# Kernel tuning notes

Hardware: AMD Instinct MI355X
Metric: run time of the kernel (lower is better)

The kernel has to match this reference:

```python
import jax, jax.numpy as jnp
import numpy as np

B, K, DIM = 8192, 256, 1024


def setup_inputs() -> dict:
    key = jax.random.key(0)
    k1, k2, k3 = jax.random.split(key, 3)
    x = jax.random.normal(k1, (B, DIM), dtype=jnp.float32)
    centers = jax.random.uniform(k2, (K, DIM), dtype=jnp.float32)
    # torch init: D = 0.2 * rand + 0.9
    D = 0.2 * jax.random.uniform(k3, (K, DIM), dtype=jnp.float32) + 0.9
    return {"x": x, "centers": centers, "D": D}


def reference(x, centers, D):
    # Per-class axis-aligned (diagonal) covariance
    D_abs = jnp.abs(D) + 1e-4                      # [K, DIM]
    D_inv = 1.0 / D_abs                            # [K, DIM]
    log_det = jnp.sum(jnp.log(D_abs), axis=1)      # [K]
    det_scale_factor = -0.5 * log_det
    det_scale_safe = jnp.exp(det_scale_factor - jnp.max(det_scale_factor))  # [K]

    # dist_sq[b,k] = sum_d (x[b,d]-c[k,d])^2 * D_inv[k,d]
    # Expanded quadratic form avoids materializing the [B,K,DIM] diff tensor.
    x2 = jnp.einsum('bd,kd->bk', x * x, D_inv)             # [B, K]
    xc = jnp.einsum('bd,kd->bk', x, centers * D_inv)       # [B, K]
    c2 = jnp.sum(centers * centers * D_inv, axis=1)        # [K]
    dist_sq = x2 - 2.0 * xc + c2[None, :]                  # [B, K]

    # Gaussian path (isCauchy=False)
    expo = -0.5 * dist_sq
    expo_safe = expo - jnp.max(expo, axis=-1, keepdims=True)
    numer_safe = det_scale_safe[None, :] * jnp.exp(expo_safe)
    denom_safe = jnp.sum(numer_safe, axis=1, keepdims=True)
    resp = numer_safe / denom_safe                         # [B, K]
    return resp
```

## Files before the change

### kernel.cpp

```cpp
#include <hip/hip_runtime.h>

typedef _Float16 f16x8 __attribute__((ext_vector_type(8)));
typedef _Float16 f16x4 __attribute__((ext_vector_type(4)));
typedef float f32x4 __attribute__((ext_vector_type(4)));

#define B_N 8192
#define K_N 256
#define DIM_N 1024

__global__ __launch_bounds__(256) void prep_w(const float* __restrict__ Dm,
                                              const float* __restrict__ Cm,
                                              _Float16* __restrict__ Upk,
                                              _Float16* __restrict__ Wpk,
                                              float* __restrict__ ec) {
    const int k = blockIdx.x, t = threadIdx.x;
    const int d = t * 4;
    const float4 dv = *(const float4*)(Dm + (size_t)k * DIM_N + d);
    const float4 cv = *(const float4*)(Cm + (size_t)k * DIM_N + d);
    float dd[4] = {dv.x, dv.y, dv.z, dv.w};
    float cc[4] = {cv.x, cv.y, cv.z, cv.w};
    f16x4 uo, wo;
    float llog = 0.f, lc2 = 0.f;
#pragma unroll
    for (int i = 0; i < 4; ++i) {
        float da = fabsf(dd[i]) + 1e-4f;
        float dinv = 1.0f / da;
        llog += logf(da);
        lc2 += cc[i] * cc[i] * dinv;
        uo[i] = (_Float16)(dinv - 1.0f);
        wo[i] = (_Float16)(-2.0f * cc[i] * dinv);
    }
    const int cg = k >> 4, cl = k & 15;
    const int kc = d >> 5, g = (d >> 3) & 3, j0 = d & 7;
    const size_t off = ((size_t)(cg * 32 + kc) * 64 + g * 16 + cl) * 8 + j0;
    *(f16x4*)(Upk + off) = uo;
    *(f16x4*)(Wpk + off) = wo;
    float both = llog + lc2;
#pragma unroll
    for (int m = 1; m <= 32; m <<= 1) both += __shfl_xor(both, m, 64);
    __shared__ float sb[4];
    if ((t & 63) == 0) sb[t >> 6] = both;
    __syncthreads();
    if (t == 0) ec[k] = -0.5f * (sb[0] + sb[1] + sb[2] + sb[3]);
}

__global__ __launch_bounds__(256, 1)
void gmm_gemm(const float* __restrict__ x,
              const _Float16* __restrict__ Upk,
              const _Float16* __restrict__ Wpk,
              float* __restrict__ S) {
    __shared__ __align__(16) char lds[32768];

    const int tid = threadIdx.x;
    const int wave = tid >> 6, lane = tid & 63;
    const int l15 = lane & 15, g4 = lane >> 4;
    const int wr = wave >> 1, wc = wave & 1;
    const int bid = blockIdx.x;
    const int rowp = bid >> 1, colp = bid & 1;
    const int bRow = rowp * 64, bCol = colp * 128;

    const int xr = lane >> 3, xdq = lane & 7;
    const float* xp = x + (size_t)(bRow + wr * 32 + xr) * DIM_N + xdq * 4;

    const int cgb = colp * 8 + wc * 4;
    const _Float16* upb = Upk + (size_t)cgb * 32 * 512 + lane * 8;
    const _Float16* wpb = Wpk + (size_t)cgb * 32 * 512 + lane * 8;

    char* wlds = lds + wave * 8192;
    const int di = xdq >> 1, jb = (lane & 1) * 8;
    int awr[4];
#pragma unroll
    for (int i = 0; i < 4; ++i) {
        const int r = xr + 8 * i;
        awr[i] = ((r >> 4) << 10) + (((r & 15) + (di << 4)) << 4) + jb;
    }

    float4 xv[3][4];
    f16x8 ub[2][4], wb[2][4];
    f32x4 acc[2][4];
#pragma unroll
    for (int m = 0; m < 2; ++m)
#pragma unroll
        for (int n = 0; n < 4; ++n) { f32x4 z = {0.f, 0.f, 0.f, 0.f}; acc[m][n] = z; }

    auto issueB = [&](int bank, int c) {
#pragma unroll
        for (int n = 0; n < 4; ++n) {
            ub[bank][n] = *(const f16x8*)(upb + ((size_t)n * 32 + c) * 512);
            wb[bank][n] = *(const f16x8*)(wpb + ((size_t)n * 32 + c) * 512);
        }
    };
    auto issueX = [&](int slot, int c) {
#pragma unroll
        for (int i = 0; i < 4; ++i)
            xv[slot][i] = *(const float4*)(xp + (size_t)c * 32 + (size_t)i * 8 * DIM_N);
    };
    auto stageA = [&](int sel, int slot) {
        char* base = wlds + sel * 4096;
#pragma unroll
        for (int i = 0; i < 4; ++i) {
            const float f0 = xv[slot][i].x, f1 = xv[slot][i].y;
            const float f2 = xv[slot][i].z, f3 = xv[slot][i].w;
            f16x4 h2 = {(_Float16)(f0 * f0), (_Float16)(f1 * f1),
                        (_Float16)(f2 * f2), (_Float16)(f3 * f3)};
            f16x4 hx = {(_Float16)f0, (_Float16)f1, (_Float16)f2, (_Float16)f3};
            *(f16x4*)(base + awr[i]) = h2;
            *(f16x4*)(base + 2048 + awr[i]) = hx;
        }
    };
    auto compute = [&](int sel, int bank) {
        char* base = wlds + sel * 4096;
        f16x8 a2f[2], axf[2];
#pragma unroll
        for (int m = 0; m < 2; ++m) {
            a2f[m] = *(const f16x8*)(base + m * 1024 + lane * 16);
            axf[m] = *(const f16x8*)(base + 2048 + m * 1024 + lane * 16);
        }
        __builtin_amdgcn_s_setprio(1);
#pragma unroll
        for (int m = 0; m < 2; ++m)
#pragma unroll
            for (int n = 0; n < 4; ++n) {
                acc[m][n] = __builtin_amdgcn_mfma_f32_16x16x32_f16(a2f[m], ub[bank][n], acc[m][n], 0, 0, 0);
                acc[m][n] = __builtin_amdgcn_mfma_f32_16x16x32_f16(axf[m], wb[bank][n], acc[m][n], 0, 0, 0);
            }
        __builtin_amdgcn_s_setprio(0);
    };

    issueB(0, 0);
    issueX(0, 0); issueX(1, 1); issueX(2, 2);
    stageA(0, 0);

#pragma unroll
    for (int c = 0; c < 32; ++c) {
        const int sel = c & 1;
        if (c < 31) issueB(sel ^ 1, c + 1);
        if (c < 29) issueX((c + 3) % 3, c + 3);
        if (c < 31) stageA(sel ^ 1, (c + 1) % 3);
        compute(sel, sel);
    }

#pragma unroll
    for (int m = 0; m < 2; ++m) {
        const int rb = bRow + wr * 32 + m * 16 + g4 * 4;
#pragma unroll
        for (int n = 0; n < 4; ++n) {
            const int cb = bCol + wc * 64 + n * 16 + l15;
#pragma unroll
            for (int j = 0; j < 4; ++j)
                S[(size_t)(rb + j) * K_N + cb] = acc[m][n][j];
        }
    }
}

__global__ __launch_bounds__(256)
void gmm_soft(float* __restrict__ S, const float* __restrict__ ecg) {
    const int tid = threadIdx.x;
    const int wave = tid >> 6, lane = tid & 63;
    const int r = blockIdx.x * 4 + wave;
    const int k0 = lane * 4;
    float4 s = *(const float4*)(S + (size_t)r * K_N + k0);
    float4 cv = *(const float4*)(ecg + k0);
    float e[4] = {fmaf(-0.5f, s.x, cv.x), fmaf(-0.5f, s.y, cv.y),
                  fmaf(-0.5f, s.z, cv.z), fmaf(-0.5f, s.w, cv.w)};
    float m = fmaxf(fmaxf(e[0], e[1]), fmaxf(e[2], e[3]));
#pragma unroll
    for (int msk = 1; msk <= 32; msk <<= 1) m = fmaxf(m, __shfl_xor(m, msk, 64));
    float p[4], sum = 0.f;
#pragma unroll
    for (int j = 0; j < 4; ++j) {
        p[j] = __expf(e[j] - m);
        sum += p[j];
    }
#pragma unroll
    for (int msk = 1; msk <= 32; msk <<= 1) sum += __shfl_xor(sum, msk, 64);
    const float inv = 1.0f / sum;
    *(float4*)(S + (size_t)r * K_N + k0) = make_float4(p[0] * inv, p[1] * inv, p[2] * inv, p[3] * inv);
}

extern "C" void kernel_launch(void* const* d_in, const int* in_sizes, int n_in,
                              void* d_out, int out_size, void* d_ws, size_t ws_size,
                              hipStream_t stream) {
    const float* x = (const float*)d_in[0];
    const float* cen = (const float*)d_in[1];
    const float* Dm = (const float*)d_in[2];
    float* out = (float*)d_out;

    char* ws = (char*)d_ws;
    _Float16* Upk = (_Float16*)(ws);
    _Float16* Wpk = (_Float16*)(ws + 524288);
    float* ec = (float*)(ws + 1048576);

    prep_w<<<dim3(K_N), dim3(256), 0, stream>>>(Dm, cen, Upk, Wpk, ec);
    gmm_gemm<<<dim3(256), dim3(256), 0, stream>>>(x, Upk, Wpk, out);
    gmm_soft<<<dim3(B_N / 4), dim3(256), 0, stream>>>(out, ec);
}
```

Baseline: 36.25 us.

## Fuse GEMM and softmax into one kernel with full-row tiles per block

```diff
diff --git a/kernel.cpp b/kernel.cpp
--- a/kernel.cpp
+++ b/kernel.cpp
@@ -44,138 +44,195 @@
     if (t == 0) ec[k] = -0.5f * (sb[0] + sb[1] + sb[2] + sb[3]);
 }
 
-__global__ __launch_bounds__(256, 1)
-void gmm_gemm(const float* __restrict__ x,
-              const _Float16* __restrict__ Upk,
-              const _Float16* __restrict__ Wpk,
-              float* __restrict__ S) {
-    __shared__ __align__(16) char lds[32768];
+__global__ __launch_bounds__(512, 1)
+void gmm_fused(const float* __restrict__ x,
+               const _Float16* __restrict__ Upk,
+               const _Float16* __restrict__ Wpk,
+               const float* __restrict__ ecg,
+               float* __restrict__ out) {
+    __shared__ __align__(16) char lds[16384];
+    __shared__ float red[8][32];
 
     const int tid = threadIdx.x;
     const int wave = tid >> 6, lane = tid & 63;
     const int l15 = lane & 15, g4 = lane >> 4;
-    const int wr = wave >> 1, wc = wave & 1;
-    const int bid = blockIdx.x;
-    const int rowp = bid >> 1, colp = bid & 1;
-    const int bRow = rowp * 64, bCol = colp * 128;
-
-    const int xr = lane >> 3, xdq = lane & 7;
-    const float* xp = x + (size_t)(bRow + wr * 32 + xr) * DIM_N + xdq * 4;
-
-    const int cgb = colp * 8 + wc * 4;
-    const _Float16* upb = Upk + (size_t)cgb * 32 * 512 + lane * 8;
-    const _Float16* wpb = Wpk + (size_t)cgb * 32 * 512 + lane * 8;
-
-    char* wlds = lds + wave * 8192;
-    const int di = xdq >> 1, jb = (lane & 1) * 8;
-    int awr[4];
-#pragma unroll
-    for (int i = 0; i < 4; ++i) {
-        const int r = xr + 8 * i;
-        awr[i] = ((r >> 4) << 10) + (((r & 15) + (di << 4)) << 4) + jb;
-    }
-
-    float4 xv[3][4];
-    f16x8 ub[2][4], wb[2][4];
-    f32x4 acc[2][4];
-#pragma unroll
-    for (int m = 0; m < 2; ++m)
-#pragma unroll
-        for (int n = 0; n < 4; ++n) { f32x4 z = {0.f, 0.f, 0.f, 0.f}; acc[m][n] = z; }
-
+    const int bRow = blockIdx.x * 32;
+
+    const int srow = tid >> 4, sdg = tid & 15;
+    const float* xp = x + (size_t)(bRow + srow) * DIM_N + sdg * 4;
+    const int wByte = srow * 128 + ((((sdg >> 1) ^ (srow & 7)) << 4) | ((sdg & 1) << 3));
+
+    const _Float16* upb = Upk + (size_t)(wave * 2) * 32 * 512 + lane * 8;
+    const _Float16* wpb = Wpk + (size_t)(wave * 2) * 32 * 512 + lane * 8;
+
+    int aRd[2][2];
+#pragma unroll
+    for (int m = 0; m < 2; ++m)
+#pragma unroll
+        for (int k2 = 0; k2 < 2; ++k2) {
+            const int row = m * 16 + l15;
+            aRd[m][k2] = row * 128 + ((((k2 * 4 + g4) ^ (row & 7)) << 4));
+        }
+
+    f32x4 acc[2][2];
+#pragma unroll
+    for (int m = 0; m < 2; ++m)
+#pragma unroll
+        for (int n = 0; n < 2; ++n) { f32x4 z = {0.f, 0.f, 0.f, 0.f}; acc[m][n] = z; }
+
+    float4 xv[6];
+    f16x8 ub[2][2][2], wb[2][2][2];
+
+    auto issueX = [&](int slot, int c) { xv[slot] = *(const float4*)(xp + c * 64); };
     auto issueB = [&](int bank, int c) {
 #pragma unroll
-        for (int n = 0; n < 4; ++n) {
-            ub[bank][n] = *(const f16x8*)(upb + ((size_t)n * 32 + c) * 512);
-            wb[bank][n] = *(const f16x8*)(wpb + ((size_t)n * 32 + c) * 512);
-        }
+        for (int n = 0; n < 2; ++n)
+#pragma unroll
+            for (int k2 = 0; k2 < 2; ++k2) {
+                const int kc = c * 2 + k2;
+                ub[bank][n][k2] = *(const f16x8*)(upb + (size_t)(n * 32 + kc) * 512);
+                wb[bank][n][k2] = *(const f16x8*)(wpb + (size_t)(n * 32 + kc) * 512);
+            }
     };
-    auto issueX = [&](int slot, int c) {
-#pragma unroll
-        for (int i = 0; i < 4; ++i)
-            xv[slot][i] = *(const float4*)(xp + (size_t)c * 32 + (size_t)i * 8 * DIM_N);
-    };
-    auto stageA = [&](int sel, int slot) {
-        char* base = wlds + sel * 4096;
-#pragma unroll
-        for (int i = 0; i < 4; ++i) {
-            const float f0 = xv[slot][i].x, f1 = xv[slot][i].y;
-            const float f2 = xv[slot][i].z, f3 = xv[slot][i].w;
-            f16x4 h2 = {(_Float16)(f0 * f0), (_Float16)(f1 * f1),
-                        (_Float16)(f2 * f2), (_Float16)(f3 * f3)};
-            f16x4 hx = {(_Float16)f0, (_Float16)f1, (_Float16)f2, (_Float16)f3};
-            *(f16x4*)(base + awr[i]) = h2;
-            *(f16x4*)(base + 2048 + awr[i]) = hx;
-        }
+    auto stage = [&](int sel, int slot) {
+        char* base = lds + sel * 8192;
+        const float f0 = xv[slot].x, f1 = xv[slot].y, f2 = xv[slot].z, f3 = xv[slot].w;
+        f16x4 h2 = {(_Float16)(f0 * f0), (_Float16)(f1 * f1),
+                    (_Float16)(f2 * f2), (_Float16)(f3 * f3)};
+        f16x4 hx = {(_Float16)f0, (_Float16)f1, (_Float16)f2, (_Float16)f3};
+        *(f16x4*)(base + wByte) = h2;
+        *(f16x4*)(base + 4096 + wByte) = hx;
     };
     auto compute = [&](int sel, int bank) {
-        char* base = wlds + sel * 4096;
-        f16x8 a2f[2], axf[2];
-#pragma unroll
-        for (int m = 0; m < 2; ++m) {
-            a2f[m] = *(const f16x8*)(base + m * 1024 + lane * 16);
-            axf[m] = *(const f16x8*)(base + 2048 + m * 1024 + lane * 16);
-        }
+        char* base = lds + sel * 8192;
+        f16x8 a2f[2][2], axf[2][2];
+#pragma unroll
+        for (int m = 0; m < 2; ++m)
+#pragma unroll
+            for (int k2 = 0; k2 < 2; ++k2) {
+                a2f[m][k2] = *(const f16x8*)(base + aRd[m][k2]);
+                axf[m][k2] = *(const f16x8*)(base + 4096 + aRd[m][k2]);
+            }
         __builtin_amdgcn_s_setprio(1);
 #pragma unroll
         for (int m = 0; m < 2; ++m)
 #pragma unroll
-            for (int n = 0; n < 4; ++n) {
-                acc[m][n] = __builtin_amdgcn_mfma_f32_16x16x32_f16(a2f[m], ub[bank][n], acc[m][n], 0, 0, 0);
-                acc[m][n] = __builtin_amdgcn_mfma_f32_16x16x32_f16(axf[m], wb[bank][n], acc[m][n], 0, 0, 0);
-            }
+            for (int n = 0; n < 2; ++n)
+#pragma unroll
+                for (int k2 = 0; k2 < 2; ++k2) {
+                    acc[m][n] = __builtin_amdgcn_mfma_f32_16x16x32_f16(a2f[m][k2], ub[bank][n][k2], acc[m][n], 0, 0, 0);
+                    acc[m][n] = __builtin_amdgcn_mfma_f32_16x16x32_f16(axf[m][k2], wb[bank][n][k2], acc[m][n], 0, 0, 0);
+                }
         __builtin_amdgcn_s_setprio(0);
     };
 
     issueB(0, 0);
-    issueX(0, 0); issueX(1, 1); issueX(2, 2);
-    stageA(0, 0);
-
-#pragma unroll
-    for (int c = 0; c < 32; ++c) {
+    issueB(1, 1);
+#pragma unroll
+    for (int s = 0; s < 6; ++s) issueX(s, s);
+    stage(0, 0);
+    asm volatile("s_waitcnt lgkmcnt(0)" ::: "memory");
+    __builtin_amdgcn_s_barrier();
+    __builtin_amdgcn_sched_barrier(0);
+
+#pragma unroll
+    for (int c = 0; c < 16; ++c) {
         const int sel = c & 1;
-        if (c < 31) issueB(sel ^ 1, c + 1);
-        if (c < 29) issueX((c + 3) % 3, c + 3);
-        if (c < 31) stageA(sel ^ 1, (c + 1) % 3);
+        if (c < 10) issueX(c % 6, c + 6);
+        if (c < 15) stage(sel ^ 1, (c + 1) % 6);
         compute(sel, sel);
-    }
-
-#pragma unroll
-    for (int m = 0; m < 2; ++m) {
-        const int rb = bRow + wr * 32 + m * 16 + g4 * 4;
-#pragma unroll
-        for (int n = 0; n < 4; ++n) {
-            const int cb = bCol + wc * 64 + n * 16 + l15;
+        if (c < 14) issueB(sel, c + 2);
+        if (c < 15) {
+            asm volatile("s_waitcnt lgkmcnt(0)" ::: "memory");
+            __builtin_amdgcn_s_barrier();
+            __builtin_amdgcn_sched_barrier(0);
+        }
+    }
+
+    const int cls0 = wave * 32 + l15;
+    const float ecv[2] = {ecg[cls0], ecg[cls0 + 16]};
+
+    float e[2][2][4];
+#pragma unroll
+    for (int m = 0; m < 2; ++m)
+#pragma unroll
+        for (int n = 0; n < 2; ++n)
 #pragma unroll
             for (int j = 0; j < 4; ++j)
-                S[(size_t)(rb + j) * K_N + cb] = acc[m][n][j];
-        }
-    }
-}
-
-__global__ __launch_bounds__(256)
-void gmm_soft(float* __restrict__ S, const float* __restrict__ ecg) {
-    const int tid = threadIdx.x;
-    const int wave = tid >> 6, lane = tid & 63;
-    const int r = blockIdx.x * 4 + wave;
-    const int k0 = lane * 4;
-    float4 s = *(const float4*)(S + (size_t)r * K_N + k0);
-    float4 cv = *(const float4*)(ecg + k0);
-    float e[4] = {fmaf(-0.5f, s.x, cv.x), fmaf(-0.5f, s.y, cv.y),
-                  fmaf(-0.5f, s.z, cv.z), fmaf(-0.5f, s.w, cv.w)};
-    float m = fmaxf(fmaxf(e[0], e[1]), fmaxf(e[2], e[3]));
-#pragma unroll
-    for (int msk = 1; msk <= 32; msk <<= 1) m = fmaxf(m, __shfl_xor(m, msk, 64));
-    float p[4], sum = 0.f;
-#pragma unroll
-    for (int j = 0; j < 4; ++j) {
-        p[j] = __expf(e[j] - m);
-        sum += p[j];
-    }
-#pragma unroll
-    for (int msk = 1; msk <= 32; msk <<= 1) sum += __shfl_xor(sum, msk, 64);
-    const float inv = 1.0f / sum;
-    *(float4*)(S + (size_t)r * K_N + k0) = make_float4(p[0] * inv, p[1] * inv, p[2] * inv, p[3] * inv);
+                e[m][n][j] = fmaf(-0.5f, acc[m][n][j], ecv[n]);
+
+    float mx[2][4];
+#pragma unroll
+    for (int m = 0; m < 2; ++m)
+#pragma unroll
+        for (int j = 0; j < 4; ++j) mx[m][j] = fmaxf(e[m][0][j], e[m][1][j]);
+#pragma unroll
+    for (int msk = 1; msk <= 8; msk <<= 1)
+#pragma unroll
+        for (int m = 0; m < 2; ++m)
+#pragma unroll
+            for (int j = 0; j < 4; ++j)
+                mx[m][j] = fmaxf(mx[m][j], __shfl_xor(mx[m][j], msk, 64));
+    if (l15 == 0) {
+#pragma unroll
+        for (int m = 0; m < 2; ++m)
+#pragma unroll
+            for (int j = 0; j < 4; ++j) red[wave][m * 16 + g4 * 4 + j] = mx[m][j];
+    }
+    __syncthreads();
+    float gm[2][4];
+#pragma unroll
+    for (int m = 0; m < 2; ++m)
+#pragma unroll
+        for (int j = 0; j < 4; ++j) {
+            const int r = m * 16 + g4 * 4 + j;
+            float v = red[0][r];
+#pragma unroll
+            for (int w = 1; w < 8; ++w) v = fmaxf(v, red[w][r]);
+            gm[m][j] = v;
+        }
+    __syncthreads();
+
+    float p[2][2][4], sm[2][4];
+#pragma unroll
+    for (int m = 0; m < 2; ++m)
+#pragma unroll
+        for (int j = 0; j < 4; ++j) sm[m][j] = 0.f;
+#pragma unroll
+    for (int m = 0; m < 2; ++m)
+#pragma unroll
+        for (int n = 0; n < 2; ++n)
+#pragma unroll
+            for (int j = 0; j < 4; ++j) {
+                p[m][n][j] = __expf(e[m][n][j] - gm[m][j]);
+                sm[m][j] += p[m][n][j];
+            }
+#pragma unroll
+    for (int msk = 1; msk <= 8; msk <<= 1)
+#pragma unroll
+        for (int m = 0; m < 2; ++m)
+#pragma unroll
+            for (int j = 0; j < 4; ++j) sm[m][j] += __shfl_xor(sm[m][j], msk, 64);
+    if (l15 == 0) {
+#pragma unroll
+        for (int m = 0; m < 2; ++m)
+#pragma unroll
+            for (int j = 0; j < 4; ++j) red[wave][m * 16 + g4 * 4 + j] = sm[m][j];
+    }
+    __syncthreads();
+#pragma unroll
+    for (int m = 0; m < 2; ++m)
+#pragma unroll
+        for (int j = 0; j < 4; ++j) {
+            const int r = m * 16 + g4 * 4 + j;
+            float t = red[0][r];
+#pragma unroll
+            for (int w = 1; w < 8; ++w) t += red[w][r];
+            const float inv = 1.0f / t;
+#pragma unroll
+            for (int n = 0; n < 2; ++n)
+                out[(size_t)(bRow + r) * K_N + cls0 + n * 16] = p[m][n][j] * inv;
+        }
 }
 
 extern "C" void kernel_launch(void* const* d_in, const int* in_sizes, int n_in,
@@ -192,6 +249,5 @@
     float* ec = (float*)(ws + 1048576);
 
     prep_w<<<dim3(K_N), dim3(256), 0, stream>>>(Dm, cen, Upk, Wpk, ec);
-    gmm_gemm<<<dim3(256), dim3(256), 0, stream>>>(x, Upk, Wpk, out);
-    gmm_soft<<<dim3(B_N / 4), dim3(256), 0, stream>>>(out, ec);
+    gmm_fused<<<dim3(B_N / 32), dim3(512), 0, stream>>>(x, Upk, Wpk, ec, out);
 }
```

Result: faster. 31.79 us (-12.3%).

## Share cooperatively staged x tiles across 8 waves with block-wide LDS pipeline

Applied to the files above, without the earlier changes.

```diff
diff --git a/kernel.cpp b/kernel.cpp
--- a/kernel.cpp
+++ b/kernel.cpp
@@ -44,111 +44,135 @@
     if (t == 0) ec[k] = -0.5f * (sb[0] + sb[1] + sb[2] + sb[3]);
 }
 
-__global__ __launch_bounds__(256, 1)
+__global__ __launch_bounds__(512, 1)
 void gmm_gemm(const float* __restrict__ x,
               const _Float16* __restrict__ Upk,
               const _Float16* __restrict__ Wpk,
               float* __restrict__ S) {
-    __shared__ __align__(16) char lds[32768];
+    __shared__ __align__(16) char xlds[65536];
 
     const int tid = threadIdx.x;
     const int wave = tid >> 6, lane = tid & 63;
     const int l15 = lane & 15, g4 = lane >> 4;
-    const int wr = wave >> 1, wc = wave & 1;
+    const int wr = wave >> 2, wc = wave & 3;
     const int bid = blockIdx.x;
-    const int rowp = bid >> 1, colp = bid & 1;
+    const int rowp = bid & 127, colp = bid >> 7;
     const int bRow = rowp * 64, bCol = colp * 128;
 
-    const int xr = lane >> 3, xdq = lane & 7;
-    const float* xp = x + (size_t)(bRow + wr * 32 + xr) * DIM_N + xdq * 4;
-
-    const int cgb = colp * 8 + wc * 4;
-    const _Float16* upb = Upk + (size_t)cgb * 32 * 512 + lane * 8;
-    const _Float16* wpb = Wpk + (size_t)cgb * 32 * 512 + lane * 8;
-
-    char* wlds = lds + wave * 8192;
-    const int di = xdq >> 1, jb = (lane & 1) * 8;
-    int awr[4];
-#pragma unroll
-    for (int i = 0; i < 4; ++i) {
-        const int r = xr + 8 * i;
-        awr[i] = ((r >> 4) << 10) + (((r & 15) + (di << 4)) << 4) + jb;
-    }
-
-    float4 xv[3][4];
-    f16x8 ub[2][4], wb[2][4];
-    f32x4 acc[2][4];
+    const int sr = tid >> 3, q4 = tid & 7;
+    const float* xq = x + (size_t)(bRow + sr) * DIM_N + q4 * 4;
+    int wAddr[8];
+#pragma unroll
+    for (int j = 0; j < 8; ++j) {
+        const int cl = j >> 1, k2 = j & 1;
+        const int fi = (sr >> 4) * 2 + k2;
+        wAddr[j] = cl * 8192 + fi * 1024 + ((sr & 15) + 16 * (q4 >> 1)) * 16 + (q4 & 1) * 8;
+    }
+
+    const _Float16* upb = Upk + (size_t)(colp * 8 + wc * 2) * 32 * 512 + lane * 8;
+    const _Float16* wpb = Wpk + (size_t)(colp * 8 + wc * 2) * 32 * 512 + lane * 8;
+
+    f32x4 acc[2][2];
 #pragma unroll
     for (int m = 0; m < 2; ++m)
 #pragma unroll
-        for (int n = 0; n < 4; ++n) { f32x4 z = {0.f, 0.f, 0.f, 0.f}; acc[m][n] = z; }
-
+        for (int n = 0; n < 2; ++n) { f32x4 z = {0.f, 0.f, 0.f, 0.f}; acc[m][n] = z; }
+
+    float4 xs[2][8];
+    f16x8 ub[2][2][2], wb[2][2][2];
+
+    auto issueQ = [&](int bank, int q) {
+#pragma unroll
+        for (int j = 0; j < 8; ++j) xs[bank][j] = *(const float4*)(xq + q * 256 + j * 32);
+    };
+    auto writeQ = [&](int bank, int buf) {
+        char* base = xlds + buf * 32768;
+#pragma unroll
+        for (int j = 0; j < 8; ++j) {
+            const float4 v = xs[bank][j];
+            f16x4 h = {(_Float16)v.x, (_Float16)v.y, (_Float16)v.z, (_Float16)v.w};
+            *(f16x4*)(base + wAddr[j]) = h;
+        }
+    };
     auto issueB = [&](int bank, int c) {
 #pragma unroll
-        for (int n = 0; n < 4; ++n) {
-            ub[bank][n] = *(const f16x8*)(upb + ((size_t)n * 32 + c) * 512);
-            wb[bank][n] = *(const f16x8*)(wpb + ((size_t)n * 32 + c) * 512);
-        }
-    };
-    auto issueX = [&](int slot, int c) {
-#pragma unroll
-        for (int i = 0; i < 4; ++i)
-            xv[slot][i] = *(const float4*)(xp + (size_t)c * 32 + (size_t)i * 8 * DIM_N);
-    };
-    auto stageA = [&](int sel, int slot) {
-        char* base = wlds + sel * 4096;
-#pragma unroll
-        for (int i = 0; i < 4; ++i) {
-            const float f0 = xv[slot][i].x, f1 = xv[slot][i].y;
-            const float f2 = xv[slot][i].z, f3 = xv[slot][i].w;
-            f16x4 h2 = {(_Float16)(f0 * f0), (_Float16)(f1 * f1),
-                        (_Float16)(f2 * f2), (_Float16)(f3 * f3)};
-            f16x4 hx = {(_Float16)f0, (_Float16)f1, (_Float16)f2, (_Float16)f3};
-            *(f16x4*)(base + awr[i]) = h2;
-            *(f16x4*)(base + 2048 + awr[i]) = hx;
-        }
-    };
-    auto compute = [&](int sel, int bank) {
-        char* base = wlds + sel * 4096;
-        f16x8 a2f[2], axf[2];
-#pragma unroll
-        for (int m = 0; m < 2; ++m) {
-            a2f[m] = *(const f16x8*)(base + m * 1024 + lane * 16);
-            axf[m] = *(const f16x8*)(base + 2048 + m * 1024 + lane * 16);
-        }
-        __builtin_amdgcn_s_setprio(1);
+        for (int n = 0; n < 2; ++n)
+#pragma unroll
+            for (int k2 = 0; k2 < 2; ++k2) {
+                const int kc = c * 2 + k2;
+                ub[bank][n][k2] = *(const f16x8*)(upb + (size_t)(n * 32 + kc) * 512);
+                wb[bank][n][k2] = *(const f16x8*)(wpb + (size_t)(n * 32 + kc) * 512);
+            }
+    };
+    auto compute = [&](int c, int bank) {
+        const char* base = xlds + ((c >> 2) & 1) * 32768 + (c & 3) * 8192;
+        f16x8 axf[2][2];
 #pragma unroll
         for (int m = 0; m < 2; ++m)
 #pragma unroll
-            for (int n = 0; n < 4; ++n) {
-                acc[m][n] = __builtin_amdgcn_mfma_f32_16x16x32_f16(a2f[m], ub[bank][n], acc[m][n], 0, 0, 0);
-                acc[m][n] = __builtin_amdgcn_mfma_f32_16x16x32_f16(axf[m], wb[bank][n], acc[m][n], 0, 0, 0);
+            for (int k2 = 0; k2 < 2; ++k2) {
+                const int fi = (wr * 2 + m) * 2 + k2;
+                axf[m][k2] = *(const f16x8*)(base + fi * 1024 + lane * 16);
             }
-        __builtin_amdgcn_s_setprio(0);
-    };
-
-    issueB(0, 0);
-    issueX(0, 0); issueX(1, 1); issueX(2, 2);
-    stageA(0, 0);
-
-#pragma unroll
-    for (int c = 0; c < 32; ++c) {
-        const int sel = c & 1;
-        if (c < 31) issueB(sel ^ 1, c + 1);
-        if (c < 29) issueX((c + 3) % 3, c + 3);
-        if (c < 31) stageA(sel ^ 1, (c + 1) % 3);
-        compute(sel, sel);
-    }
+#pragma unroll
+        for (int m = 0; m < 2; ++m)
+#pragma unroll
+            for (int k2 = 0; k2 < 2; ++k2) {
+                const f16x8 a2 = axf[m][k2] * axf[m][k2];
+#pragma unroll
+                for (int n = 0; n < 2; ++n) {
+                    acc[m][n] = __builtin_amdgcn_mfma_f32_16x16x32_f16(a2, ub[bank][n][k2], acc[m][n], 0, 0, 0);
+                    acc[m][n] = __builtin_amdgcn_mfma_f32_16x16x32_f16(axf[m][k2], wb[bank][n][k2], acc[m][n], 0, 0, 0);
+                }
+            }
+    };
+
+    issueB(0, 0); issueB(1, 1);
+    issueQ(0, 0); issueQ(1, 1);
+    writeQ(0, 0);
+    asm volatile("s_waitcnt lgkmcnt(0)" ::: "memory");
+    __builtin_amdgcn_s_barrier();
+    __builtin_amdgcn_sched_barrier(0);
+    writeQ(1, 1);
+    issueQ(0, 2);
+    compute(0, 0);  issueB(0, 2);
+    compute(1, 1);  issueB(1, 3);
+    compute(2, 0);  issueB(0, 4);
+    compute(3, 1);  issueB(1, 5);
+    asm volatile("s_waitcnt lgkmcnt(0)" ::: "memory");
+    __builtin_amdgcn_s_barrier();
+    __builtin_amdgcn_sched_barrier(0);
+    writeQ(0, 0);
+    issueQ(1, 3);
+    compute(4, 0);  issueB(0, 6);
+    compute(5, 1);  issueB(1, 7);
+    compute(6, 0);  issueB(0, 8);
+    compute(7, 1);  issueB(1, 9);
+    asm volatile("s_waitcnt lgkmcnt(0)" ::: "memory");
+    __builtin_amdgcn_s_barrier();
+    __builtin_amdgcn_sched_barrier(0);
+    writeQ(1, 1);
+    compute(8, 0);   issueB(0, 10);
+    compute(9, 1);   issueB(1, 11);
+    compute(10, 0);  issueB(0, 12);
+    compute(11, 1);  issueB(1, 13);
+    asm volatile("s_waitcnt lgkmcnt(0)" ::: "memory");
+    __builtin_amdgcn_s_barrier();
+    __builtin_amdgcn_sched_barrier(0);
+    compute(12, 0);  issueB(0, 14);
+    compute(13, 1);  issueB(1, 15);
+    compute(14, 0);
+    compute(15, 1);
 
 #pragma unroll
     for (int m = 0; m < 2; ++m) {
         const int rb = bRow + wr * 32 + m * 16 + g4 * 4;
-#pragma unroll
-        for (int n = 0; n < 4; ++n) {
-            const int cb = bCol + wc * 64 + n * 16 + l15;
-#pragma unroll
-            for (int j = 0; j < 4; ++j)
-                S[(size_t)(rb + j) * K_N + cb] = acc[m][n][j];
+        const int cb = bCol + wc * 32 + l15;
+#pragma unroll
+        for (int j = 0; j < 4; ++j) {
+            float* p = S + (size_t)(rb + j) * K_N + cb;
+            p[0] = acc[m][0][j];
+            p[16] = acc[m][1][j];
         }
     }
 }
@@ -192,6 +216,6 @@
     float* ec = (float*)(ws + 1048576);
 
     prep_w<<<dim3(K_N), dim3(256), 0, stream>>>(Dm, cen, Upk, Wpk, ec);
-    gmm_gemm<<<dim3(256), dim3(256), 0, stream>>>(x, Upk, Wpk, out);
+    gmm_gemm<<<dim3(256), dim3(512), 0, stream>>>(x, Upk, Wpk, out);
     gmm_soft<<<dim3(B_N / 4), dim3(256), 0, stream>>>(out, ec);
 }
```

Result: faster. 32.65 us (-9.9%).
